# Optimization experiments

Hardware: AMD Instinct MI355X
Metric: run time of the kernel (lower is better)

## Reference

```python
import jax, jax.numpy as jnp
import numpy as np

B, H, W, C, NH, WS, SS = 16, 112, 112, 384, 12, 7, 3
HD = C // NH          # head dim = 32
N = WS * WS           # tokens per window = 49
MLP_H = 4 * C         # 1536
NW = (H // WS) * (W // WS)  # windows per image = 256


def _rel_pos_index():
    coords = np.stack(np.meshgrid(np.arange(WS), np.arange(WS), indexing='ij')).reshape(2, -1)
    rel = (coords[:, :, None] - coords[:, None, :]).transpose(1, 2, 0)  # (N, N, 2)
    rel[..., 0] += WS - 1
    rel[..., 1] += WS - 1
    rel[..., 0] *= 2 * WS - 1
    return rel.sum(-1)  # (N, N) in [0, (2WS-1)^2)


def _attn_mask():
    img = np.zeros((H, W))
    cnt = 0
    slices = (slice(0, -WS), slice(-WS, -SS), slice(-SS, None))
    for hs in slices:
        for ws_ in slices:
            img[hs, ws_] = cnt
            cnt += 1
    mw = img.reshape(H // WS, WS, W // WS, WS).transpose(0, 2, 1, 3).reshape(-1, N)
    am = mw[:, None, :] - mw[:, :, None]
    return np.where(am != 0, -100.0, 0.0).astype(np.float32)  # (NW, N, N)


REL_IDX = jnp.asarray(_rel_pos_index().reshape(-1))  # (N*N,) int
MASK = jnp.asarray(_attn_mask())                      # (NW, N, N)


def _ln(x, g, b, eps=1e-5):
    m = jnp.mean(x, -1, keepdims=True)
    v = jnp.mean((x - m) ** 2, -1, keepdims=True)
    return (x - m) / jnp.sqrt(v + eps) * g + b


def setup_inputs() -> dict:
    key = jax.random.key(0)
    ks = jax.random.split(key, 16)
    s = 0.02
    return {
        'x': jax.random.normal(ks[0], (B, H * W, C), jnp.float32),
        'norm1_g': jnp.ones((C,), jnp.float32),
        'norm1_b': jnp.zeros((C,), jnp.float32),
        'qkv_w': jax.random.normal(ks[1], (C, 3 * C), jnp.float32) * s,
        'qkv_b': jnp.zeros((3 * C,), jnp.float32),
        'proj_w': jax.random.normal(ks[2], (C, C), jnp.float32) * s,
        'proj_b': jnp.zeros((C,), jnp.float32),
        'rpb_table': jax.random.normal(ks[3], ((2 * WS - 1) ** 2, NH), jnp.float32) * s,
        'norm2_g': jnp.ones((C,), jnp.float32),
        'norm2_b': jnp.zeros((C,), jnp.float32),
        'fc1_w': jax.random.normal(ks[4], (C, MLP_H), jnp.float32) * s,
        'fc1_b': jnp.zeros((MLP_H,), jnp.float32),
        'fc2_w': jax.random.normal(ks[5], (MLP_H, C), jnp.float32) * s,
        'fc2_b': jnp.zeros((C,), jnp.float32),
    }


def reference(x, norm1_g, norm1_b, qkv_w, qkv_b, proj_w, proj_b, rpb_table,
              norm2_g, norm2_b, fc1_w, fc1_b, fc2_w, fc2_b):
    shortcut = x
    h = _ln(x, norm1_g, norm1_b).reshape(B, H, W, C)
    # cyclic shift
    h = jnp.roll(h, (-SS, -SS), axis=(1, 2))
    # window partition -> (B*NW, N, C)
    wins = h.reshape(B, H // WS, WS, W // WS, WS, C).transpose(0, 1, 3, 2, 4, 5).reshape(-1, N, C)
    qkv = (wins @ qkv_w + qkv_b).reshape(-1, N, 3, NH, HD).transpose(2, 0, 3, 1, 4)
    q, k, v = qkv[0] * HD ** -0.5, qkv[1], qkv[2]  # (B*NW, NH, N, HD)
    attn = jnp.einsum('bhnd,bhmd->bhnm', q, k)
    bias = rpb_table[REL_IDX].reshape(N, N, NH).transpose(2, 0, 1)  # (NH, N, N)
    attn = attn + bias[None]
    attn = (attn.reshape(B, NW, NH, N, N) + MASK[None, :, None]).reshape(-1, NH, N, N)
    attn = jax.nn.softmax(attn, axis=-1)
    out = jnp.einsum('bhnm,bhmd->bhnd', attn, v).transpose(0, 2, 1, 3).reshape(-1, N, C)
    out = out @ proj_w + proj_b
    # window reverse
    out = out.reshape(B, H // WS, W // WS, WS, WS, C).transpose(0, 1, 3, 2, 4, 5).reshape(B, H, W, C)
    out = jnp.roll(out, (SS, SS), axis=(1, 2)).reshape(B, H * W, C)
    x = shortcut + out
    h2 = _ln(x, norm2_g, norm2_b)
    h2 = jax.nn.gelu(h2 @ fc1_w + fc1_b, approximate=False) @ fc2_w + fc2_b
    return x + h2
```

## Files before the change

kernel.cpp:

```cpp
#include <hip/hip_runtime.h>
#include <hip/hip_bf16.h>

typedef short bf16x8 __attribute__((ext_vector_type(8)));
typedef float f32x4 __attribute__((ext_vector_type(4)));
typedef float f32x16 __attribute__((ext_vector_type(16)));
typedef unsigned int u32x4 __attribute__((ext_vector_type(4)));

typedef __attribute__((address_space(1))) void gvoid;
typedef __attribute__((address_space(3))) void lvoid;

__device__ __forceinline__ short f2b(float f) {
  __hip_bfloat16 h = __float2bfloat16(f);
  return __builtin_bit_cast(short, h);
}

__device__ __forceinline__ f32x4 mfma16(bf16x8 a, bf16x8 b, f32x4 c) {
  return __builtin_amdgcn_mfma_f32_16x16x32_bf16(a, b, c, 0, 0, 0);
}

__device__ __forceinline__ f32x16 mfma32(bf16x8 a, bf16x8 b, f32x16 c) {
  return __builtin_amdgcn_mfma_f32_32x32x16_bf16(a, b, c, 0, 0, 0);
}

__device__ __forceinline__ unsigned cvtpk(float lo, float hi) {
  unsigned r;
  asm("v_cvt_pk_bf16_f32 %0, %1, %2" : "=v"(r) : "v"(lo), "v"(hi));
  return r;
}

__device__ __forceinline__ void gload16(const void* g, void* l) {
  __builtin_amdgcn_global_load_lds((const gvoid*)g, (lvoid*)l, 16, 0, 0);
}

__global__ __launch_bounds__(256) void convT_k(const float* __restrict__ src,
                                               short* __restrict__ dst, int K,
                                               int N, int scale_cols,
                                               float scale) {
  int idx = blockIdx.x * 256 + threadIdx.x;
  if (idx >= N * K) return;
  int n = idx / K, k = idx % K;
  float v = src[(size_t)k * N + n];
  if (n < scale_cols) v *= scale;
  dst[idx] = f2b(v);
}

__global__ __launch_bounds__(256) void scale_bias_k(const float* __restrict__ src,
                                                    float* __restrict__ dst,
                                                    int n, int scale_cols,
                                                    float scale) {
  int i = blockIdx.x * 256 + threadIdx.x;
  if (i >= n) return;
  dst[i] = src[i] * (i < scale_cols ? scale : 1.f);
}

__global__ __launch_bounds__(256) void biasmask_k(const float* __restrict__ rpb,
                                                  float* __restrict__ tbl) {
  int idx = blockIdx.x * 256 + threadIdx.x;
  int q = idx & 63, key = (idx >> 6) & 63;
  int hc = idx >> 12;
  int h = hc % 12, cls = hc / 12;
  float v;
  if (q >= 49 || key >= 49) {
    v = -1e4f;
  } else {
    int i1 = q / 7, j1 = q % 7, i2 = key / 7, j2 = key % 7;
    v = rpb[(size_t)((i1 - i2 + 6) * 13 + (j1 - j2 + 6)) * 12 + h];
    int clsh = cls >> 1, clsw = cls & 1;
    int rq = (clsh ? 1 + (i1 >= 4) : 0) * 3 + (clsw ? 1 + (j1 >= 4) : 0);
    int rk = (clsh ? 1 + (i2 >= 4) : 0) * 3 + (clsw ? 1 + (j2 >= 4) : 0);
    if (rq != rk) v -= 100.f;
  }
  tbl[idx] = v;
}

template <bool GATHER>
__device__ __forceinline__ void ln_body(const float* __restrict__ x,
                                        const float* __restrict__ gw,
                                        const float* __restrict__ bw,
                                        short* __restrict__ out) {
  const int lane = threadIdx.x & 63;
  const int t = (blockIdx.x << 2) + (threadIdx.x >> 6);
  size_t srow;
  if (GATHER) {
    int bb = t / 12544, rm2 = t % 12544;
    int wi = rm2 / 49, nn = rm2 % 49;
    int wh = wi >> 4, ww = wi & 15;
    int ii = nn / 7, jj = nn % 7;
    int rr = wh * 7 + ii + 3; if (rr >= 112) rr -= 112;
    int cc = ww * 7 + jj + 3; if (cc >= 112) cc -= 112;
    srow = ((size_t)bb * 12544 + rr * 112 + cc) * 384;
  } else {
    srow = (size_t)t * 384;
  }
  const float2* src = (const float2*)(x + srow);
  const float2* g2 = (const float2*)gw;
  const float2* b2 = (const float2*)bw;
  float2 u[3];
  float s = 0.f, ss = 0.f;
#pragma unroll
  for (int k = 0; k < 3; ++k) {
    u[k] = src[lane + (k << 6)];
    s += u[k].x + u[k].y;
    ss += u[k].x * u[k].x + u[k].y * u[k].y;
  }
#pragma unroll
  for (int m = 1; m < 64; m <<= 1) {
    s += __shfl_xor(s, m, 64);
    ss += __shfl_xor(ss, m, 64);
  }
  const float mean = s * (1.f / 384.f);
  const float var = ss * (1.f / 384.f) - mean * mean;
  const float rstd = rsqrtf(var + 1e-5f);
  unsigned* o = (unsigned*)(out + (size_t)t * 384);
#pragma unroll
  for (int k = 0; k < 3; ++k) {
    int c = lane + (k << 6);
    float2 gv = g2[c], bv = b2[c];
    unsigned lo = (unsigned short)f2b((u[k].x - mean) * rstd * gv.x + bv.x);
    unsigned hi = (unsigned short)f2b((u[k].y - mean) * rstd * gv.y + bv.y);
    o[c] = lo | (hi << 16);
  }
}

__global__ __launch_bounds__(256) void ln1_k(const float* __restrict__ x,
                                             const float* __restrict__ gw,
                                             const float* __restrict__ bw,
                                             short* __restrict__ out) {
  ln_body<true>(x, gw, bw, out);
}
__global__ __launch_bounds__(256) void ln2_k(const float* __restrict__ x,
                                             const float* __restrict__ gw,
                                             const float* __restrict__ bw,
                                             short* __restrict__ out) {
  ln_body<false>(x, gw, bw, out);
}

template <int EPI>
__device__ __forceinline__ void gemm_body(
    const short* __restrict__ A, int lda, const short* __restrict__ BT,
    int ldb, const float* __restrict__ bias, int K, short* __restrict__ outh,
    int ldo, float* __restrict__ outf, const float* __restrict__ resid) {
  __shared__ __align__(16) short A0[4096], B0[4096];
  __shared__ __align__(16) short A1[4096], B1[4096];
  __shared__ __align__(16) short A2[4096], B2[4096];
  const int tid = threadIdx.x;
  const int gx = gridDim.x;
  int lin = blockIdx.y * gx + blockIdx.x;
  const int cpx = (gx * gridDim.y) >> 3;
  lin = (lin & 7) * cpx + (lin >> 3);
  const int m0 = (lin / gx) << 7, n0 = (lin % gx) << 7;
  const int lane = tid & 63;
  const int wave = tid >> 6;
  const int wr = (wave >> 1) << 6, wc = (wave & 1) << 6;
  const int g = lane >> 4, q = lane & 15;
  const int loff = tid << 3;

  f32x4 acc[4][4];
#pragma unroll
  for (int i = 0; i < 4; ++i)
#pragma unroll
    for (int j = 0; j < 4; ++j) acc[i][j] = (f32x4){0.f, 0.f, 0.f, 0.f};

  const short* Ab = A + (size_t)(m0 + (tid >> 2)) * lda + ((tid & 3) << 3);
  const short* Ab2 = Ab + (size_t)64 * lda;
  const short* Bb = BT + (size_t)(n0 + (tid >> 2)) * ldb + ((tid & 3) << 3);
  const short* Bb2 = Bb + (size_t)64 * ldb;

#define STAGE(kt, dA, dB)                   \
  do {                                      \
    gload16(Ab + (kt), &dA[loff]);          \
    gload16(Ab2 + (kt), &dA[loff + 2048]);  \
    gload16(Bb + (kt), &dB[loff]);          \
    gload16(Bb2 + (kt), &dB[loff + 2048]);  \
  } while (0)

#define COMPUTE(SA, SB)                                               \
  do {                                                                \
    bf16x8 af[4], bfv[4];                                             \
    _Pragma("unroll") for (int mi = 0; mi < 4; ++mi)                  \
        af[mi] = *(const bf16x8*)&SA[(wr + mi * 16 + q) * 32 + g * 8];\
    _Pragma("unroll") for (int ni = 0; ni < 4; ++ni)                  \
        bfv[ni] = *(const bf16x8*)&SB[(wc + ni * 16 + q) * 32 + g * 8];\
    _Pragma("unroll") for (int mi = 0; mi < 4; ++mi)                  \
        _Pragma("unroll") for (int ni = 0; ni < 4; ++ni)              \
            acc[mi][ni] = mfma16(af[mi], bfv[ni], acc[mi][ni]);       \
  } while (0)

#define VM4                                           \
  do {                                                \
    asm volatile("s_waitcnt vmcnt(4)" ::: "memory");  \
    __builtin_amdgcn_sched_barrier(0);                \
  } while (0)
#define VM0                                           \
  do {                                                \
    asm volatile("s_waitcnt vmcnt(0)" ::: "memory");  \
    __builtin_amdgcn_sched_barrier(0);                \
  } while (0)
#define BAR __builtin_amdgcn_s_barrier()

  const int nt = K >> 5;
  STAGE(0, A0, B0);
  STAGE(32, A1, B1);
  VM4;
  BAR;
  int kk = 64;
  for (int t = 0; t + 3 < nt; t += 3) {
    STAGE(kk, A2, B2);
    COMPUTE(A0, B0);
    VM4;
    BAR;
    STAGE(kk + 32, A0, B0);
    COMPUTE(A1, B1);
    VM4;
    BAR;
    STAGE(kk + 64, A1, B1);
    COMPUTE(A2, B2);
    VM4;
    BAR;
    kk += 96;
  }
  STAGE(kk, A2, B2);
  COMPUTE(A0, B0);
  VM4;
  BAR;
  COMPUTE(A1, B1);
  VM0;
  BAR;
  COMPUTE(A2, B2);
#undef STAGE
#undef COMPUTE
#undef VM4
#undef VM0
#undef BAR

  float bv[4];
#pragma unroll
  for (int ni = 0; ni < 4; ++ni)
    bv[ni] = bias ? bias[n0 + wc + ni * 16 + q] : 0.f;

#pragma unroll
  for (int mi = 0; mi < 4; ++mi) {
#pragma unroll
    for (int r = 0; r < 4; ++r) {
      const int grow = m0 + wr + mi * 16 + g * 4 + r;
      size_t orow;
      if constexpr (EPI == 2) {
        int bb = grow / 12544, rm2 = grow % 12544;
        int wi = rm2 / 49, nn = rm2 % 49;
        int wh = wi >> 4, ww = wi & 15;
        int ii = nn / 7, jj = nn % 7;
        int rr = wh * 7 + ii + 3; if (rr >= 112) rr -= 112;
        int cc = ww * 7 + jj + 3; if (cc >= 112) cc -= 112;
        orow = ((size_t)bb * 12544 + rr * 112 + cc) * 384;
      } else {
        orow = (size_t)grow * (size_t)ldo;
      }
#pragma unroll
      for (int ni = 0; ni < 4; ++ni) {
        const int gcol = n0 + wc + ni * 16 + q;
        float v = acc[mi][ni][r] + bv[ni];
        if constexpr (EPI == 0) {
          outh[orow + gcol] = f2b(v);
        } else if constexpr (EPI == 1) {
          v = 0.5f * v * (1.f + erff(v * 0.70710678118f));
          outh[orow + gcol] = f2b(v);
        } else if constexpr (EPI == 2) {
          outf[orow + gcol] = resid[orow + gcol] + v;
        } else {
          outf[orow + gcol] += v;
        }
      }
    }
  }
}

#define GEMM_WRAP(NAME, EPI)                                                   \
  __global__ __launch_bounds__(256) void NAME(                                 \
      const short* __restrict__ A, int lda, const short* __restrict__ BT,      \
      int ldb, const float* __restrict__ bias, int K,                          \
      short* __restrict__ outh, int ldo, float* __restrict__ outf,             \
      const float* __restrict__ resid) {                                       \
    gemm_body<EPI>(A, lda, BT, ldb, bias, K, outh, ldo, outf, resid);          \
  }
GEMM_WRAP(gemm_qkv_k, 0)
GEMM_WRAP(gemm_fc1_k, 1)
GEMM_WRAP(gemm_proj_k, 2)
GEMM_WRAP(gemm_fc2_k, 3)

__global__ __launch_bounds__(256) void attn_k(const short* __restrict__ qkv,
                                              const float* __restrict__ tbl,
                                              short* __restrict__ out) {
  const int lane = threadIdx.x & 63;
  const int task = blockIdx.x * 4 + (threadIdx.x >> 6);
  const int win = task / 12;
  const int h = task - win * 12;
  const int wh = (win >> 4) & 15, ww = win & 15;
  const int cls = ((wh == 15) ? 2 : 0) + ((ww == 15) ? 1 : 0);
  const int l31 = lane & 31, h5 = lane >> 5;
  const size_t tokbase = (size_t)win * 49;
  const short* base = qkv + tokbase * 1152 + h * 32;
  const bf16x8 zero8 = {0, 0, 0, 0, 0, 0, 0, 0};

  bf16x8 kf[2][2];
#pragma unroll
  for (int mi = 0; mi < 2; ++mi) {
    int row = l31 + 32 * mi;
#pragma unroll
    for (int s = 0; s < 2; ++s)
      kf[mi][s] = (row < 49)
                      ? *(const bf16x8*)(base + (size_t)row * 1152 + 384 +
                                         16 * s + 8 * h5)
                      : zero8;
  }
  bf16x8 vf[4];
#pragma unroll
  for (int kt = 0; kt < 4; ++kt) {
#pragma unroll
    for (int e = 0; e < 8; ++e) {
      int key = 16 * kt + 8 * h5 + e;
      vf[kt][e] = (key < 49) ? base[(size_t)key * 1152 + 768 + l31] : (short)0;
    }
  }

  const float* tb = tbl + ((size_t)(cls * 12 + h) << 12);

#pragma unroll
  for (int ni = 0; ni < 2; ++ni) {
    bf16x8 qf[2];
    int qrow = l31 + 32 * ni;
#pragma unroll
    for (int s = 0; s < 2; ++s)
      qf[s] = (qrow < 49)
                  ? *(const bf16x8*)(base + (size_t)qrow * 1152 + 16 * s +
                                     8 * h5)
                  : zero8;
    f32x16 st[2];
#pragma unroll
    for (int mi = 0; mi < 2; ++mi) {
      st[mi] = mfma32(kf[mi][0], qf[0], (f32x16)(0.f));
      st[mi] = mfma32(kf[mi][1], qf[1], st[mi]);
    }
#pragma unroll
    for (int mi = 0; mi < 2; ++mi)
#pragma unroll
      for (int r = 0; r < 16; ++r) {
        int koff = (r & 3) + 8 * (r >> 2) + 4 * h5;
        st[mi][r] += tb[(size_t)(32 * mi + koff) * 64 + 32 * ni + l31];
      }
    float mx = st[0][0];
#pragma unroll
    for (int r = 1; r < 16; ++r) mx = fmaxf(mx, st[0][r]);
#pragma unroll
    for (int r = 0; r < 16; ++r) mx = fmaxf(mx, st[1][r]);
    mx = fmaxf(mx, __shfl_xor(mx, 32, 64));
    float sm = 0.f;
#pragma unroll
    for (int mi = 0; mi < 2; ++mi)
#pragma unroll
      for (int r = 0; r < 16; ++r) {
        float e = __expf(st[mi][r] - mx);
        st[mi][r] = e;
        sm += e;
      }
    sm += __shfl_xor(sm, 32, 64);
    const float rinv = 1.f / sm;
#pragma unroll
    for (int mi = 0; mi < 2; ++mi)
#pragma unroll
      for (int r = 0; r < 16; ++r) st[mi][r] *= rinv;

    f32x16 acc = (f32x16)(0.f);
#pragma unroll
    for (int kt = 0; kt < 4; ++kt) {
      const int mi = kt >> 1, b8 = (kt & 1) * 8;
      unsigned q0l = cvtpk(st[mi][b8 + 0], st[mi][b8 + 1]);
      unsigned q0h = cvtpk(st[mi][b8 + 2], st[mi][b8 + 3]);
      unsigned q1l = cvtpk(st[mi][b8 + 4], st[mi][b8 + 5]);
      unsigned q1h = cvtpk(st[mi][b8 + 6], st[mi][b8 + 7]);
      unsigned sl = h5 ? q0l : q1l, sh = h5 ? q0h : q1h;
      unsigned kl = h5 ? q1l : q0l, kh = h5 ? q1h : q0h;
      unsigned rl = (unsigned)__shfl_xor((int)sl, 32, 64);
      unsigned rh = (unsigned)__shfl_xor((int)sh, 32, 64);
      u32x4 fr;
      fr[0] = h5 ? rl : kl;
      fr[1] = h5 ? rh : kh;
      fr[2] = h5 ? kl : rl;
      fr[3] = h5 ? kh : rh;
      acc = mfma32(__builtin_bit_cast(bf16x8, fr), vf[kt], acc);
    }
#pragma unroll
    for (int r = 0; r < 16; ++r) {
      int query = 32 * ni + (r & 3) + 8 * (r >> 2) + 4 * h5;
      if (ni == 0 || query < 49)
        out[(tokbase + query) * 384 + h * 32 + l31] = f2b(acc[r]);
    }
  }
}

extern "C" void kernel_launch(void* const* d_in, const int* in_sizes, int n_in,
                              void* d_out, int out_size, void* d_ws,
                              size_t ws_size, hipStream_t stream) {
  const float* x = (const float*)d_in[0];
  const float* n1g = (const float*)d_in[1];
  const float* n1b = (const float*)d_in[2];
  const float* qkvw = (const float*)d_in[3];
  const float* qkvb = (const float*)d_in[4];
  const float* projw = (const float*)d_in[5];
  const float* projb = (const float*)d_in[6];
  const float* rpb = (const float*)d_in[7];
  const float* n2g = (const float*)d_in[8];
  const float* n2b = (const float*)d_in[9];
  const float* fc1w = (const float*)d_in[10];
  const float* fc1b = (const float*)d_in[11];
  const float* fc2w = (const float*)d_in[12];
  const float* fc2b = (const float*)d_in[13];
  float* out = (float*)d_out;

  char* ws = (char*)d_ws;
  short* w_qkvT = (short*)(ws + 0);
  short* w_projT = (short*)(ws + 884736);
  short* w_fc1T = (short*)(ws + 1179648);
  short* w_fc2T = (short*)(ws + 2359296);
  float* w_qb = (float*)(ws + 3538944);
  float* tbl = (float*)(ws + 3543552);
  const size_t o_qkv = 4329984;
  short* qkvbuf = (short*)(ws + o_qkv);
  const size_t o_hwin = o_qkv + 462422016ull;
  short* hwin = (short*)(ws + o_hwin);
  const size_t o_fc1 = o_hwin + 154140672ull;

  int NC;
  size_t fc1_off = o_fc1;
  if (ws_size >= o_fc1 + 616562688ull) NC = 1;
  else if (ws_size >= o_fc1 + 308281344ull) NC = 2;
  else if (ws_size >= o_fc1 + 154140672ull) NC = 4;
  else { NC = 4; fc1_off = o_hwin; }
  short* fc1c = (short*)(ws + fc1_off);
  short* h2 = qkvbuf;

  const float qscale = 0.17677669529663687f;

  convT_k<<<(442368 + 255) / 256, 256, 0, stream>>>(qkvw, w_qkvT, 384, 1152, 384, qscale);
  convT_k<<<(147456 + 255) / 256, 256, 0, stream>>>(projw, w_projT, 384, 384, 0, 1.f);
  convT_k<<<(589824 + 255) / 256, 256, 0, stream>>>(fc1w, w_fc1T, 384, 1536, 0, 1.f);
  convT_k<<<(589824 + 255) / 256, 256, 0, stream>>>(fc2w, w_fc2T, 1536, 384, 0, 1.f);
  scale_bias_k<<<5, 256, 0, stream>>>(qkvb, w_qb, 1152, 384, qscale);
  biasmask_k<<<768, 256, 0, stream>>>(rpb, tbl);

  ln1_k<<<50176, 256, 0, stream>>>(x, n1g, n1b, hwin);
  gemm_qkv_k<<<dim3(9, 1568), 256, 0, stream>>>(hwin, 384, w_qkvT, 384, w_qb,
                                                384, qkvbuf, 1152, nullptr,
                                                nullptr);
  attn_k<<<12288, 256, 0, stream>>>(qkvbuf, tbl, hwin);
  gemm_proj_k<<<dim3(3, 1568), 256, 0, stream>>>(hwin, 384, w_projT, 384,
                                                 projb, 384, nullptr, 384, out,
                                                 x);
  ln2_k<<<50176, 256, 0, stream>>>(out, n2g, n2b, h2);
  const int CK = 1536 / NC;
  for (int c = 0; c < NC; ++c) {
    gemm_fc1_k<<<dim3(CK >> 7, 1568), 256, 0, stream>>>(
        h2, 384, w_fc1T + (size_t)c * CK * 384, 384, fc1b + c * CK, 384, fc1c,
        CK, nullptr, nullptr);
    gemm_fc2_k<<<dim3(3, 1568), 256, 0, stream>>>(
        fc1c, CK, w_fc2T + c * CK, 1536, (c == 0) ? fc2b : nullptr, CK,
        nullptr, 384, out, nullptr);
  }
}
```

Baseline: 2.176 ms.

## Switch GEMMs to 256x128 tiles with 32x32 MFMA, swizzled LDS, vector epilogue

Doubles the GEMM M-tile to 256 rows and halves the grid. Each wave now computes a 128x64 sub-tile using 32x32x16 bf16 MFMAs instead of 16x16x32, which raises arithmetic intensity per LDS read. LDS chunks are XOR-swizzled to avoid bank conflicts, and the epilogue writes 4-wide vectorized bf16/fp32 stores with packed conversion. The cost is more accumulator registers and LDS per block, which may lower occupancy.

```diff
diff --git a/kernel.cpp b/kernel.cpp
--- a/kernel.cpp
+++ b/kernel.cpp
@@ -5,6 +5,7 @@
 typedef float f32x4 __attribute__((ext_vector_type(4)));
 typedef float f32x16 __attribute__((ext_vector_type(16)));
 typedef unsigned int u32x4 __attribute__((ext_vector_type(4)));
+typedef unsigned int u32x2 __attribute__((ext_vector_type(2)));
 
 typedef __attribute__((address_space(1))) void gvoid;
 typedef __attribute__((address_space(3))) void lvoid;
@@ -12,10 +13,6 @@
 __device__ __forceinline__ short f2b(float f) {
   __hip_bfloat16 h = __float2bfloat16(f);
   return __builtin_bit_cast(short, h);
-}
-
-__device__ __forceinline__ f32x4 mfma16(bf16x8 a, bf16x8 b, f32x4 c) {
-  return __builtin_amdgcn_mfma_f32_16x16x32_bf16(a, b, c, 0, 0, 0);
 }
 
 __device__ __forceinline__ f32x16 mfma32(bf16x8 a, bf16x8 b, f32x16 c) {
@@ -140,55 +137,70 @@
     const short* __restrict__ A, int lda, const short* __restrict__ BT,
     int ldb, const float* __restrict__ bias, int K, short* __restrict__ outh,
     int ldo, float* __restrict__ outf, const float* __restrict__ resid) {
-  __shared__ __align__(16) short A0[4096], B0[4096];
-  __shared__ __align__(16) short A1[4096], B1[4096];
-  __shared__ __align__(16) short A2[4096], B2[4096];
+  __shared__ __align__(16) short A0s[8192], B0s[4096];
+  __shared__ __align__(16) short A1s[8192], B1s[4096];
+  __shared__ __align__(16) short A2s[8192], B2s[4096];
   const int tid = threadIdx.x;
   const int gx = gridDim.x;
   int lin = blockIdx.y * gx + blockIdx.x;
   const int cpx = (gx * gridDim.y) >> 3;
   lin = (lin & 7) * cpx + (lin >> 3);
-  const int m0 = (lin / gx) << 7, n0 = (lin % gx) << 7;
+  const int m0 = (lin / gx) << 8, n0 = (lin % gx) << 7;
   const int lane = tid & 63;
   const int wave = tid >> 6;
-  const int wr = (wave >> 1) << 6, wc = (wave & 1) << 6;
-  const int g = lane >> 4, q = lane & 15;
+  const int wr = (wave >> 1) << 7, wc = (wave & 1) << 6;
+  const int l31 = lane & 31, h5 = (lane >> 5) & 1;
   const int loff = tid << 3;
-
-  f32x4 acc[4][4];
+  const int cswz = (tid & 3) ^ ((tid >> 3) & 3);
+  const int cperm = (l31 >> 1) & 3;
+  const int co0 = ((h5) ^ cperm) << 3;
+  const int co1 = ((2 + h5) ^ cperm) << 3;
+  const int ia0 = (wr + l31) * 32 + co0;
+  const int ia1 = (wr + l31) * 32 + co1;
+  const int ib0 = (wc + l31) * 32 + co0;
+  const int ib1 = (wc + l31) * 32 + co1;
+
+  f32x16 acc[4][2];
 #pragma unroll
   for (int i = 0; i < 4; ++i)
 #pragma unroll
-    for (int j = 0; j < 4; ++j) acc[i][j] = (f32x4){0.f, 0.f, 0.f, 0.f};
-
-  const short* Ab = A + (size_t)(m0 + (tid >> 2)) * lda + ((tid & 3) << 3);
-  const short* Ab2 = Ab + (size_t)64 * lda;
-  const short* Bb = BT + (size_t)(n0 + (tid >> 2)) * ldb + ((tid & 3) << 3);
-  const short* Bb2 = Bb + (size_t)64 * ldb;
-
-#define STAGE(kt, dA, dB)                   \
-  do {                                      \
-    gload16(Ab + (kt), &dA[loff]);          \
-    gload16(Ab2 + (kt), &dA[loff + 2048]);  \
-    gload16(Bb + (kt), &dB[loff]);          \
-    gload16(Bb2 + (kt), &dB[loff + 2048]);  \
+    for (int j = 0; j < 2; ++j) acc[i][j] = (f32x16)(0.f);
+
+  const short* Ab = A + (size_t)(m0 + (tid >> 2)) * lda + cswz * 8;
+  const short* Bb = BT + (size_t)(n0 + (tid >> 2)) * ldb + cswz * 8;
+  const size_t la64 = (size_t)64 * lda, lb64 = (size_t)64 * ldb;
+
+#define STAGE(kt, DA, DB)                             \
+  do {                                                \
+    gload16(Ab + (kt), &DA[loff]);                    \
+    gload16(Ab + la64 + (kt), &DA[loff + 2048]);      \
+    gload16(Ab + 2 * la64 + (kt), &DA[loff + 4096]);  \
+    gload16(Ab + 3 * la64 + (kt), &DA[loff + 6144]);  \
+    gload16(Bb + (kt), &DB[loff]);                    \
+    gload16(Bb + lb64 + (kt), &DB[loff + 2048]);      \
   } while (0)
 
-#define COMPUTE(SA, SB)                                               \
-  do {                                                                \
-    bf16x8 af[4], bfv[4];                                             \
-    _Pragma("unroll") for (int mi = 0; mi < 4; ++mi)                  \
-        af[mi] = *(const bf16x8*)&SA[(wr + mi * 16 + q) * 32 + g * 8];\
-    _Pragma("unroll") for (int ni = 0; ni < 4; ++ni)                  \
-        bfv[ni] = *(const bf16x8*)&SB[(wc + ni * 16 + q) * 32 + g * 8];\
-    _Pragma("unroll") for (int mi = 0; mi < 4; ++mi)                  \
-        _Pragma("unroll") for (int ni = 0; ni < 4; ++ni)              \
-            acc[mi][ni] = mfma16(af[mi], bfv[ni], acc[mi][ni]);       \
+#define COMPUTE(SA, SB)                                                  \
+  do {                                                                   \
+    bf16x8 af[4][2], bfr[2][2];                                          \
+    _Pragma("unroll") for (int mi = 0; mi < 4; ++mi) {                   \
+      af[mi][0] = *(const bf16x8*)&SA[ia0 + mi * 1024];                  \
+      af[mi][1] = *(const bf16x8*)&SA[ia1 + mi * 1024];                  \
+    }                                                                    \
+    _Pragma("unroll") for (int ni = 0; ni < 2; ++ni) {                   \
+      bfr[ni][0] = *(const bf16x8*)&SB[ib0 + ni * 1024];                 \
+      bfr[ni][1] = *(const bf16x8*)&SB[ib1 + ni * 1024];                 \
+    }                                                                    \
+    _Pragma("unroll") for (int mi = 0; mi < 4; ++mi)                     \
+        _Pragma("unroll") for (int ni = 0; ni < 2; ++ni) {               \
+      acc[mi][ni] = mfma32(bfr[ni][0], af[mi][0], acc[mi][ni]);          \
+      acc[mi][ni] = mfma32(bfr[ni][1], af[mi][1], acc[mi][ni]);          \
+    }                                                                    \
   } while (0)
 
-#define VM4                                           \
+#define VM6                                           \
   do {                                                \
-    asm volatile("s_waitcnt vmcnt(4)" ::: "memory");  \
+    asm volatile("s_waitcnt vmcnt(6)" ::: "memory");  \
     __builtin_amdgcn_sched_barrier(0);                \
   } while (0)
 #define VM0                                           \
@@ -199,75 +211,92 @@
 #define BAR __builtin_amdgcn_s_barrier()
 
   const int nt = K >> 5;
-  STAGE(0, A0, B0);
-  STAGE(32, A1, B1);
-  VM4;
+  STAGE(0, A0s, B0s);
+  STAGE(32, A1s, B1s);
+  VM6;
   BAR;
   int kk = 64;
   for (int t = 0; t + 3 < nt; t += 3) {
-    STAGE(kk, A2, B2);
-    COMPUTE(A0, B0);
-    VM4;
+    STAGE(kk, A2s, B2s);
+    COMPUTE(A0s, B0s);
+    VM6;
     BAR;
-    STAGE(kk + 32, A0, B0);
-    COMPUTE(A1, B1);
-    VM4;
+    STAGE(kk + 32, A0s, B0s);
+    COMPUTE(A1s, B1s);
+    VM6;
     BAR;
-    STAGE(kk + 64, A1, B1);
-    COMPUTE(A2, B2);
-    VM4;
+    STAGE(kk + 64, A1s, B1s);
+    COMPUTE(A2s, B2s);
+    VM6;
     BAR;
     kk += 96;
   }
-  STAGE(kk, A2, B2);
-  COMPUTE(A0, B0);
-  VM4;
+  STAGE(kk, A2s, B2s);
+  COMPUTE(A0s, B0s);
+  VM6;
   BAR;
-  COMPUTE(A1, B1);
+  COMPUTE(A1s, B1s);
   VM0;
   BAR;
-  COMPUTE(A2, B2);
+  COMPUTE(A2s, B2s);
 #undef STAGE
 #undef COMPUTE
-#undef VM4
+#undef VM6
 #undef VM0
 #undef BAR
 
-  float bv[4];
-#pragma unroll
-  for (int ni = 0; ni < 4; ++ni)
-    bv[ni] = bias ? bias[n0 + wc + ni * 16 + q] : 0.f;
+  f32x4 bq[2][4];
+#pragma unroll
+  for (int ni = 0; ni < 2; ++ni)
+#pragma unroll
+    for (int rg = 0; rg < 4; ++rg)
+      bq[ni][rg] = bias
+                       ? *(const f32x4*)&bias[n0 + wc + ni * 32 + rg * 8 + 4 * h5]
+                       : (f32x4){0.f, 0.f, 0.f, 0.f};
 
 #pragma unroll
   for (int mi = 0; mi < 4; ++mi) {
-#pragma unroll
-    for (int r = 0; r < 4; ++r) {
-      const int grow = m0 + wr + mi * 16 + g * 4 + r;
-      size_t orow;
-      if constexpr (EPI == 2) {
-        int bb = grow / 12544, rm2 = grow % 12544;
-        int wi = rm2 / 49, nn = rm2 % 49;
-        int wh = wi >> 4, ww = wi & 15;
-        int ii = nn / 7, jj = nn % 7;
-        int rr = wh * 7 + ii + 3; if (rr >= 112) rr -= 112;
-        int cc = ww * 7 + jj + 3; if (cc >= 112) cc -= 112;
-        orow = ((size_t)bb * 12544 + rr * 112 + cc) * 384;
-      } else {
-        orow = (size_t)grow * (size_t)ldo;
-      }
-#pragma unroll
-      for (int ni = 0; ni < 4; ++ni) {
-        const int gcol = n0 + wc + ni * 16 + q;
-        float v = acc[mi][ni][r] + bv[ni];
+    const int m = m0 + wr + mi * 32 + l31;
+    size_t orow;
+    if constexpr (EPI == 2) {
+      int bb = m / 12544, rm2 = m % 12544;
+      int wi = rm2 / 49, nn = rm2 % 49;
+      int wh = wi >> 4, ww = wi & 15;
+      int ii = nn / 7, jj = nn % 7;
+      int rr = wh * 7 + ii + 3; if (rr >= 112) rr -= 112;
+      int cc = ww * 7 + jj + 3; if (cc >= 112) cc -= 112;
+      orow = ((size_t)bb * 12544 + rr * 112 + cc) * 384;
+    } else {
+      orow = (size_t)m * (size_t)ldo;
+    }
+#pragma unroll
+    for (int ni = 0; ni < 2; ++ni) {
+#pragma unroll
+      for (int rg = 0; rg < 4; ++rg) {
+        const int col = n0 + wc + ni * 32 + rg * 8 + 4 * h5;
+        float v[4];
+#pragma unroll
+        for (int j = 0; j < 4; ++j)
+          v[j] = acc[mi][ni][rg * 4 + j] + bq[ni][rg][j];
         if constexpr (EPI == 0) {
-          outh[orow + gcol] = f2b(v);
+          u32x2 u = {cvtpk(v[0], v[1]), cvtpk(v[2], v[3])};
+          *(u32x2*)&outh[orow + col] = u;
         } else if constexpr (EPI == 1) {
-          v = 0.5f * v * (1.f + erff(v * 0.70710678118f));
-          outh[orow + gcol] = f2b(v);
+#pragma unroll
+          for (int j = 0; j < 4; ++j)
+            v[j] = 0.5f * v[j] * (1.f + erff(v[j] * 0.70710678118f));
+          u32x2 u = {cvtpk(v[0], v[1]), cvtpk(v[2], v[3])};
+          *(u32x2*)&outh[orow + col] = u;
         } else if constexpr (EPI == 2) {
-          outf[orow + gcol] = resid[orow + gcol] + v;
+          f32x4 r = *(const f32x4*)&resid[orow + col];
+#pragma unroll
+          for (int j = 0; j < 4; ++j) r[j] += v[j];
+          *(f32x4*)&outf[orow + col] = r;
         } else {
-          outf[orow + gcol] += v;
+          f32x4 o = *(f32x4*)&outf[orow + col];
+#pragma unroll
+          for (int j = 0; j < 4; ++j) o[j] += v[j];
+          *(f32x4*)&outf[orow + col] = o;
         }
       }
     }
@@ -448,20 +477,20 @@
   biasmask_k<<<768, 256, 0, stream>>>(rpb, tbl);
 
   ln1_k<<<50176, 256, 0, stream>>>(x, n1g, n1b, hwin);
-  gemm_qkv_k<<<dim3(9, 1568), 256, 0, stream>>>(hwin, 384, w_qkvT, 384, w_qb,
-                                                384, qkvbuf, 1152, nullptr,
-                                                nullptr);
+  gemm_qkv_k<<<dim3(9, 784), 256, 0, stream>>>(hwin, 384, w_qkvT, 384, w_qb,
+                                               384, qkvbuf, 1152, nullptr,
+                                               nullptr);
   attn_k<<<12288, 256, 0, stream>>>(qkvbuf, tbl, hwin);
-  gemm_proj_k<<<dim3(3, 1568), 256, 0, stream>>>(hwin, 384, w_projT, 384,
-                                                 projb, 384, nullptr, 384, out,
-                                                 x);
+  gemm_proj_k<<<dim3(3, 784), 256, 0, stream>>>(hwin, 384, w_projT, 384,
+                                                projb, 384, nullptr, 384, out,
+                                                x);
   ln2_k<<<50176, 256, 0, stream>>>(out, n2g, n2b, h2);
   const int CK = 1536 / NC;
   for (int c = 0; c < NC; ++c) {
-    gemm_fc1_k<<<dim3(CK >> 7, 1568), 256, 0, stream>>>(
+    gemm_fc1_k<<<dim3(CK >> 7, 784), 256, 0, stream>>>(
         h2, 384, w_fc1T + (size_t)c * CK * 384, 384, fc1b + c * CK, 384, fc1c,
         CK, nullptr, nullptr);
-    gemm_fc2_k<<<dim3(3, 1568), 256, 0, stream>>>(
+    gemm_fc2_k<<<dim3(3, 784), 256, 0, stream>>>(
         fc1c, CK, w_fc2T + c * CK, 1536, (c == 0) ? fc2b : nullptr, CK,
         nullptr, 384, out, nullptr);
   }
```

New measurement: 2.281 ms. 1.05x slower.
